# Kernel optimization log

Hardware: AMD Instinct MI355X
Metric: run time of the kernel (lower is better)

## Reference

```python
import jax, jax.numpy as jnp
import numpy as np

EMBED_DIM = 1024
N_HEADS = 16
D_HEAD = EMBED_DIM // N_HEADS


def setup_inputs() -> dict:
    key = jax.random.key(0)
    kx, kq, kk, kv = jax.random.split(key, 4)
    x = jax.random.normal(kx, (2, 2048, EMBED_DIM), dtype=jnp.float32)
    Wq = jax.random.normal(kq, (EMBED_DIM, EMBED_DIM), dtype=jnp.float32) * 0.02
    Wk = jax.random.normal(kk, (EMBED_DIM, EMBED_DIM), dtype=jnp.float32) * 0.02
    Wv = jax.random.normal(kv, (EMBED_DIM, EMBED_DIM), dtype=jnp.float32) * 0.02
    return {"x": x, "Wq": Wq, "Wk": Wk, "Wv": Wv}


def reference(x, Wq, Wk, Wv):
    B, N, D = x.shape
    H, Dh = N_HEADS, D_HEAD
    # Fused QKV projections, then split heads: [B, N, D] -> [B, H, N, Dh]
    q = (x @ Wq).reshape(B, N, H, Dh).transpose(0, 2, 1, 3)
    k = (x @ Wk).reshape(B, N, H, Dh).transpose(0, 2, 1, 3)
    v = (x @ Wv).reshape(B, N, H, Dh).transpose(0, 2, 1, 3)
    scale = 1.0 / jnp.sqrt(jnp.asarray(Dh, dtype=x.dtype))
    scores = jnp.einsum("bhqd,bhkd->bhqk", q, k) * scale  # [B, H, N, N]
    attn = jax.nn.softmax(scores, axis=-1)
    out = jnp.einsum("bhqk,bhkd->bhqd", attn, v)  # [B, H, N, Dh]
    return out.transpose(0, 2, 1, 3).reshape(B, N, D)
```

## Files before the change

kernel.cpp:

```cpp
#include <hip/hip_runtime.h>
#include <cstdint>

typedef __bf16 bf16;
typedef __bf16 bf16x4 __attribute__((ext_vector_type(4)));
typedef __bf16 bf16x8 __attribute__((ext_vector_type(8)));
typedef float floatx4 __attribute__((ext_vector_type(4)));

typedef const __attribute__((address_space(1))) void* as1_cvptr;
typedef __attribute__((address_space(3))) void* as3_vptr;

__device__ __forceinline__ void gl_lds16(const void* g, void* l) {
  __builtin_amdgcn_global_load_lds((as1_cvptr)(uintptr_t)g,
                                   (as3_vptr)(uint32_t)(uintptr_t)l, 16, 0, 0);
}

#define EMBED 1024
#define SEQ 2048
#define NH 16
#define DH 64
#define QSCALE 0.18033688f

__global__ __launch_bounds__(256) void prep(
    const float* __restrict__ x, const float* __restrict__ Wq,
    const float* __restrict__ Wk, const float* __restrict__ Wv,
    bf16* __restrict__ xb, bf16* __restrict__ Wqt,
    bf16* __restrict__ Wkt, bf16* __restrict__ Wvt) {
  __shared__ __align__(16) bf16 tile[64][72];
  int z = blockIdx.y;
  int t = threadIdx.x;
  if (z == 3) {
    size_t base = ((size_t)blockIdx.x * 256 + t) * 8;
#pragma unroll
    for (int it = 0; it < 8; ++it) {
      size_t i = base + (size_t)it * (256 * 256 * 8);
      floatx4 a = *(const floatx4*)(x + i);
      floatx4 bv = *(const floatx4*)(x + i + 4);
      bf16x8 o;
#pragma unroll
      for (int j = 0; j < 4; ++j) { o[j] = (bf16)a[j]; o[4 + j] = (bf16)bv[j]; }
      *(bf16x8*)(xb + i) = o;
    }
    return;
  }
  const float* W = (z == 0) ? Wq : (z == 1) ? Wk : Wv;
  bf16* Wt = (z == 0) ? Wqt : (z == 1) ? Wkt : Wvt;
  int k0 = (blockIdx.x >> 4) * 64, n0 = (blockIdx.x & 15) * 64;
  int r = t >> 3, c = (t & 7) * 8;
#pragma unroll
  for (int half = 0; half < 2; ++half) {
    const float* src = &W[(size_t)(k0 + r + half * 32) * EMBED + n0 + c];
    floatx4 f0 = *(const floatx4*)src;
    floatx4 f1 = *(const floatx4*)(src + 4);
    bf16x8 o;
#pragma unroll
    for (int j = 0; j < 4; ++j) { o[j] = (bf16)f0[j]; o[4 + j] = (bf16)f1[j]; }
    *(bf16x8*)&tile[r + half * 32][c] = o;
  }
  __syncthreads();
#pragma unroll
  for (int p = 0; p < 2; ++p) {
    int nn = (t >> 3) + p * 32, kk = (t & 7) * 8;
    bf16x8 v;
#pragma unroll
    for (int i = 0; i < 8; ++i) v[i] = tile[kk + i][nn];
    *(bf16x8*)&Wt[(size_t)(n0 + nn) * EMBED + k0 + kk] = v;
  }
}

__global__ __launch_bounds__(256) void qkv3(
    const bf16* __restrict__ Xb, const bf16* __restrict__ Wqt,
    const bf16* __restrict__ Wkt, const bf16* __restrict__ Wvt,
    bf16* __restrict__ qo, bf16* __restrict__ ko, bf16* __restrict__ vto) {
  __shared__ __align__(16) bf16 As[128 * 32];
  __shared__ __align__(16) bf16 Bs[128 * 32];

  int gid = blockIdx.x;
  int z = gid % 3;
  int rem = gid / 3;
  int bxx = rem & 7, byy = rem >> 3;

  const bf16* Wt = (z == 0) ? Wqt : (z == 1) ? Wkt : Wvt;
  bf16* out = (z == 0) ? qo : (z == 1) ? ko : vto;
  int m0 = (z == 2 ? bxx : byy) * 128;
  int n0 = (z == 2 ? byy : bxx) * 128;
  const bf16* Asrc = (z == 2) ? Wt : Xb;
  const bf16* Bsrc = (z == 2) ? Xb : Wt;
  float oscale = (z == 0) ? QSCALE : 1.0f;

  int t = threadIdx.x;
  int w = t >> 6, lane = t & 63, ln = lane & 15, quad = lane >> 4;
  int wm = (w >> 1) * 64, wn = (w & 1) * 64;

  floatx4 acc[4][4];
#pragma unroll
  for (int i = 0; i < 4; ++i)
#pragma unroll
    for (int j = 0; j < 4; ++j) acc[i][j] = floatx4{0.f, 0.f, 0.f, 0.f};

  int sr = t >> 2, sc = (t & 3) * 8;
  const bf16* ag = Asrc + (size_t)(m0 + sr) * EMBED + sc;
  const bf16* bg = Bsrc + (size_t)(n0 + sr) * EMBED + sc;
  bf16* al = As + sr * 32 + sc;
  bf16* bl = Bs + sr * 32 + sc;

  for (int k0 = 0; k0 < EMBED; k0 += 32) {
    __syncthreads();
    gl_lds16(ag + k0, al);
    gl_lds16(ag + k0 + (size_t)64 * EMBED, al + 64 * 32);
    gl_lds16(bg + k0, bl);
    gl_lds16(bg + k0 + (size_t)64 * EMBED, bl + 64 * 32);
    __syncthreads();

    bf16x8 afr[4], bfr[4];
#pragma unroll
    for (int i = 0; i < 4; ++i)
      afr[i] = *(const bf16x8*)&As[(wm + i * 16 + ln) * 32 + quad * 8];
#pragma unroll
    for (int j = 0; j < 4; ++j)
      bfr[j] = *(const bf16x8*)&Bs[(wn + j * 16 + ln) * 32 + quad * 8];
#pragma unroll
    for (int i = 0; i < 4; ++i)
#pragma unroll
      for (int j = 0; j < 4; ++j)
        acc[i][j] =
            __builtin_amdgcn_mfma_f32_16x16x32_bf16(afr[i], bfr[j], acc[i][j], 0, 0, 0);
  }

#pragma unroll
  for (int i = 0; i < 4; ++i) {
#pragma unroll
    for (int r = 0; r < 4; ++r) {
      int row = m0 + wm + i * 16 + quad * 4 + r;
#pragma unroll
      for (int j = 0; j < 4; ++j) {
        int col = n0 + wn + j * 16 + ln;
        float v = acc[i][j][r] * oscale;
        size_t dst;
        if (z != 2) {
          int b = row >> 11, ns = row & 2047, h = col >> 6, d = col & 63;
          dst = ((size_t)((b * NH + h) * SEQ + ns)) * DH + d;
        } else {
          int h = row >> 6, d = row & 63, b = col >> 11, ns = col & 2047;
          dst = ((size_t)((b * NH + h) * DH + d)) * SEQ + ns;
        }
        out[dst] = (bf16)v;
      }
    }
  }
}

__global__ __launch_bounds__(1024, 8) void flash(
    const bf16* __restrict__ Qg, const bf16* __restrict__ Kg,
    const bf16* __restrict__ Vtg, float* __restrict__ Og) {
  __shared__ __align__(16) char smem[73728];
  bf16* Ks = (bf16*)smem;
  bf16* Vs = (bf16*)(smem + 18432);
  bf16* Ps = (bf16*)(smem + 36864);
  float* Om = (float*)smem;
  float* Lm = (float*)(smem + 34816);

  int t = threadIdx.x, w = t >> 6, lane = t & 63, ln = lane & 15, quad = lane >> 4;
  int qg = w >> 1, half = w & 1;
  int bh = blockIdx.y;
  int b = bh >> 4, h = bh & 15;
  const bf16* Q = Qg + (size_t)bh * SEQ * DH;
  const bf16* K = Kg + (size_t)bh * SEQ * DH;
  const bf16* Vt = Vtg + (size_t)bh * DH * SEQ;
  int q0 = blockIdx.x * 128 + qg * 16;

  bf16x8 bq[2];
#pragma unroll
  for (int kc = 0; kc < 2; ++kc)
    bq[kc] = *(const bf16x8*)&Q[(size_t)(q0 + ln) * DH + kc * 32 + quad * 8];

  floatx4 oacc[4];
  float li = 0.f;
#pragma unroll
  for (int dt = 0; dt < 4; ++dt) oacc[dt] = floatx4{0.f, 0.f, 0.f, 0.f};

  int sh = t >> 9, st = t & 511;
  int kr = st >> 3, kcol = (st & 7) * 8;
  const bf16* kg = K + (size_t)(sh * 1024 + kr) * DH + kcol;
  const bf16* vg = Vt + (size_t)kr * SEQ + sh * 1024 + kcol;
  bf16* kl = Ks + sh * (64 * 72) + kr * 72 + kcol;
  bf16* vl = Vs + sh * (64 * 72) + kr * 72 + kcol;

  bf16x8 pk = *(const bf16x8*)(kg);
  bf16x8 pv = *(const bf16x8*)(vg);

  const bf16* Ksh = Ks + half * (64 * 72);
  const bf16* Vsh = Vs + half * (64 * 72);
  bf16* Pw = Ps + w * (16 * 72);

  for (int it = 0; it < 16; ++it) {
    __syncthreads();
    *(bf16x8*)kl = pk;
    *(bf16x8*)vl = pv;
    __syncthreads();

    if (it + 1 < 16) {
      pk = *(const bf16x8*)(kg + (size_t)((it + 1) * 64) * DH);
      pv = *(const bf16x8*)(vg + (it + 1) * 64);
    }

    floatx4 s[4];
#pragma unroll
    for (int nt = 0; nt < 4; ++nt) s[nt] = floatx4{0.f, 0.f, 0.f, 0.f};
#pragma unroll
    for (int kc = 0; kc < 2; ++kc) {
#pragma unroll
      for (int nt = 0; nt < 4; ++nt) {
        bf16x8 ak = *(const bf16x8*)&Ksh[(nt * 16 + ln) * 72 + kc * 32 + quad * 8];
        s[nt] = __builtin_amdgcn_mfma_f32_16x16x32_bf16(ak, bq[kc], s[nt], 0, 0, 0);
      }
    }

#pragma unroll
    for (int nt = 0; nt < 4; ++nt) {
      float p0 = exp2f(s[nt][0]);
      float p1 = exp2f(s[nt][1]);
      float p2 = exp2f(s[nt][2]);
      float p3 = exp2f(s[nt][3]);
      li += (p0 + p1) + (p2 + p3);
      bf16x4 pq = {(bf16)p0, (bf16)p1, (bf16)p2, (bf16)p3};
      *(bf16x4*)&Pw[ln * 72 + nt * 16 + quad * 4] = pq;
    }

#pragma unroll
    for (int kc2 = 0; kc2 < 2; ++kc2) {
      bf16x8 ap = *(const bf16x8*)&Pw[ln * 72 + kc2 * 32 + quad * 8];
#pragma unroll
      for (int dt = 0; dt < 4; ++dt) {
        bf16x8 bv = *(const bf16x8*)&Vsh[(dt * 16 + ln) * 72 + kc2 * 32 + quad * 8];
        oacc[dt] = __builtin_amdgcn_mfma_f32_16x16x32_bf16(ap, bv, oacc[dt], 0, 0, 0);
      }
    }
  }

  __syncthreads();
  li += __shfl_xor(li, 16, 64);
  li += __shfl_xor(li, 32, 64);
  if (quad == 0) Lm[half * 128 + qg * 16 + ln] = li;
  if (half) {
#pragma unroll
    for (int r = 0; r < 4; ++r) {
      int q = qg * 16 + quad * 4 + r;
#pragma unroll
      for (int dt = 0; dt < 4; ++dt) Om[q * 68 + dt * 16 + ln] = oacc[dt][r];
    }
  }
  __syncthreads();
  if (!half) {
#pragma unroll
    for (int r = 0; r < 4; ++r) {
      int qq = qg * 16 + quad * 4 + r;
      float lt = Lm[qq] + Lm[128 + qq];
      float inv = 1.0f / lt;
      int ns = blockIdx.x * 128 + qq;
#pragma unroll
      for (int dt = 0; dt < 4; ++dt) {
        int d = dt * 16 + ln;
        float val = (oacc[dt][r] + Om[qq * 68 + d]) * inv;
        Og[((size_t)(b * SEQ + ns)) * EMBED + h * DH + d] = val;
      }
    }
  }
}

extern "C" void kernel_launch(void* const* d_in, const int* in_sizes, int n_in,
                              void* d_out, int out_size, void* d_ws, size_t ws_size,
                              hipStream_t stream) {
  const int XEL = 2 * 2048 * 1024;
  const float *x, *Wq, *Wk, *Wv;
  if (in_sizes[0] == XEL) {
    x = (const float*)d_in[0];
    Wq = (const float*)d_in[1];
    Wk = (const float*)d_in[2];
    Wv = (const float*)d_in[3];
  } else {
    Wk = (const float*)d_in[0];
    Wq = (const float*)d_in[1];
    Wv = (const float*)d_in[2];
    x = (const float*)d_in[3];
  }
  bf16* ws = (bf16*)d_ws;

  const size_t M1 = 1024 * 1024;
  bf16* q_ws = ws;
  bf16* k_ws = ws + 4 * M1;
  bf16* vt_ws = ws + 8 * M1;
  bf16* wqt = ws + 12 * M1;
  bf16* wkt = ws + 13 * M1;
  bf16* wvt = ws + 14 * M1;
  bf16* xb = ws + 15 * M1;

  prep<<<dim3(256, 4), 256, 0, stream>>>(x, Wq, Wk, Wv, xb, wqt, wkt, wvt);
  qkv3<<<dim3(768), 256, 0, stream>>>(xb, wqt, wkt, wvt, q_ws, k_ws, vt_ws);
  flash<<<dim3(16, 32), 1024, 0, stream>>>(q_ws, k_ws, vt_ws, (float*)d_out);
}
```

Before: 178.2 us.

## Restructure flash kernel around 32x32x16 MFMA with in-register P and 4-way KV split

The attention kernel moves from 16x16x32 to 32x32x16 MFMA tiles. Each wave now handles 32 queries over a quarter of the key sequence. The probability tile stays in registers: it is repacked with permlane32_swap and fed straight into the PV MFMA, so the LDS round trip for P is gone. K/V tiles are double-buffered in a larger 144KB LDS block, which removes one barrier per iteration, and the four split partial outputs are reduced through LDS with vectorised final stores. The cost is lower occupancy from the larger LDS footprint and a serial three-step reduction at the end.

```diff
diff --git a/kernel.cpp b/kernel.cpp
--- a/kernel.cpp
+++ b/kernel.cpp
@@ -5,6 +5,9 @@
 typedef __bf16 bf16x4 __attribute__((ext_vector_type(4)));
 typedef __bf16 bf16x8 __attribute__((ext_vector_type(8)));
 typedef float floatx4 __attribute__((ext_vector_type(4)));
+typedef float f32x16 __attribute__((ext_vector_type(16)));
+typedef unsigned int uint2v __attribute__((ext_vector_type(2)));
+typedef unsigned int uint4v __attribute__((ext_vector_type(4)));
 
 typedef const __attribute__((address_space(1))) void* as1_cvptr;
 typedef __attribute__((address_space(3))) void* as3_vptr;
@@ -19,6 +22,12 @@
 #define NH 16
 #define DH 64
 #define QSCALE 0.18033688f
+
+__device__ __forceinline__ unsigned pk_bf16(float a, float b) {
+  unsigned short ua = __builtin_bit_cast(unsigned short, (bf16)a);
+  unsigned short ub = __builtin_bit_cast(unsigned short, (bf16)b);
+  return (unsigned)ua | ((unsigned)ub << 16);
+}
 
 __global__ __launch_bounds__(256) void prep(
     const float* __restrict__ x, const float* __restrict__ Wq,
@@ -149,121 +158,159 @@
   }
 }
 
-__global__ __launch_bounds__(1024, 8) void flash(
+__global__ __launch_bounds__(1024, 4) void flash(
     const bf16* __restrict__ Qg, const bf16* __restrict__ Kg,
     const bf16* __restrict__ Vtg, float* __restrict__ Og) {
-  __shared__ __align__(16) char smem[73728];
+  __shared__ __align__(16) char smem[147456];
   bf16* Ks = (bf16*)smem;
-  bf16* Vs = (bf16*)(smem + 18432);
-  bf16* Ps = (bf16*)(smem + 36864);
+  bf16* Vs = (bf16*)(smem + 73728);
   float* Om = (float*)smem;
   float* Lm = (float*)(smem + 34816);
 
-  int t = threadIdx.x, w = t >> 6, lane = t & 63, ln = lane & 15, quad = lane >> 4;
-  int qg = w >> 1, half = w & 1;
+  int t = threadIdx.x;
+  int lane = t & 63, w = t >> 6;
+  int col = lane & 31, hi = lane >> 5;
+  int qg = w >> 2, split = w & 3;
   int bh = blockIdx.y;
   int b = bh >> 4, h = bh & 15;
   const bf16* Q = Qg + (size_t)bh * SEQ * DH;
   const bf16* K = Kg + (size_t)bh * SEQ * DH;
   const bf16* Vt = Vtg + (size_t)bh * DH * SEQ;
-  int q0 = blockIdx.x * 128 + qg * 16;
-
-  bf16x8 bq[2];
-#pragma unroll
-  for (int kc = 0; kc < 2; ++kc)
-    bq[kc] = *(const bf16x8*)&Q[(size_t)(q0 + ln) * DH + kc * 32 + quad * 8];
-
-  floatx4 oacc[4];
+  int q0 = blockIdx.x * 128 + qg * 32;
+
+  bf16x8 bq[4];
+#pragma unroll
+  for (int kc = 0; kc < 4; ++kc)
+    bq[kc] = *(const bf16x8*)&Q[(size_t)(q0 + col) * DH + kc * 16 + hi * 8];
+
+  f32x16 oacc[2];
+#pragma unroll
+  for (int m = 0; m < 2; ++m)
+#pragma unroll
+    for (int r = 0; r < 16; ++r) oacc[m][r] = 0.f;
   float li = 0.f;
-#pragma unroll
-  for (int dt = 0; dt < 4; ++dt) oacc[dt] = floatx4{0.f, 0.f, 0.f, 0.f};
-
-  int sh = t >> 9, st = t & 511;
-  int kr = st >> 3, kcol = (st & 7) * 8;
-  const bf16* kg = K + (size_t)(sh * 1024 + kr) * DH + kcol;
-  const bf16* vg = Vt + (size_t)kr * SEQ + sh * 1024 + kcol;
-  bf16* kl = Ks + sh * (64 * 72) + kr * 72 + kcol;
-  bf16* vl = Vs + sh * (64 * 72) + kr * 72 + kcol;
-
-  bf16x8 pk = *(const bf16x8*)(kg);
-  bf16x8 pv = *(const bf16x8*)(vg);
-
-  const bf16* Ksh = Ks + half * (64 * 72);
-  const bf16* Vsh = Vs + half * (64 * 72);
-  bf16* Pw = Ps + w * (16 * 72);
-
-  for (int it = 0; it < 16; ++it) {
-    __syncthreads();
-    *(bf16x8*)kl = pk;
-    *(bf16x8*)vl = pv;
-    __syncthreads();
-
-    if (it + 1 < 16) {
-      pk = *(const bf16x8*)(kg + (size_t)((it + 1) * 64) * DH);
-      pv = *(const bf16x8*)(vg + (it + 1) * 64);
-    }
-
-    floatx4 s[4];
-#pragma unroll
-    for (int nt = 0; nt < 4; ++nt) s[nt] = floatx4{0.f, 0.f, 0.f, 0.f};
-#pragma unroll
-    for (int kc = 0; kc < 2; ++kc) {
-#pragma unroll
-      for (int nt = 0; nt < 4; ++nt) {
-        bf16x8 ak = *(const bf16x8*)&Ksh[(nt * 16 + ln) * 72 + kc * 32 + quad * 8];
-        s[nt] = __builtin_amdgcn_mfma_f32_16x16x32_bf16(ak, bq[kc], s[nt], 0, 0, 0);
+
+  int ss = t >> 8, st = t & 255;
+  int kr = st >> 2, kcol = (st & 3) * 16;
+  const bf16* kg = K + ((size_t)(ss * 512 + kr)) * DH + kcol;
+  const bf16* vg = Vt + (size_t)kr * SEQ + ss * 512 + kcol;
+  bf16* kl = Ks + ss * 4608 + kr * 72 + kcol;
+  bf16* vl = Vs + ss * 4608 + kr * 72 + kcol;
+
+  bf16x8 pk0 = *(const bf16x8*)kg;
+  bf16x8 pk1 = *(const bf16x8*)(kg + 8);
+  bf16x8 pv0 = *(const bf16x8*)vg;
+  bf16x8 pv1 = *(const bf16x8*)(vg + 8);
+
+  const bf16* Kb = Ks + split * 4608;
+  const bf16* Vb = Vs + split * 4608;
+
+  for (int it = 0; it < 8; ++it) {
+    int buf = (it & 1) * 18432;
+    *(bf16x8*)(kl + buf) = pk0;
+    *(bf16x8*)(kl + buf + 8) = pk1;
+    *(bf16x8*)(vl + buf) = pv0;
+    *(bf16x8*)(vl + buf + 8) = pv1;
+    __syncthreads();
+
+    if (it + 1 < 8) {
+      size_t ko = (size_t)(it + 1) * 64 * DH;
+      pk0 = *(const bf16x8*)(kg + ko);
+      pk1 = *(const bf16x8*)(kg + ko + 8);
+      pv0 = *(const bf16x8*)(vg + (it + 1) * 64);
+      pv1 = *(const bf16x8*)(vg + (it + 1) * 64 + 8);
+    }
+    const bf16* Kt = Kb + buf;
+    const bf16* Vtb = Vb + buf;
+
+#pragma unroll
+    for (int mt = 0; mt < 2; ++mt) {
+      f32x16 s;
+#pragma unroll
+      for (int r = 0; r < 16; ++r) s[r] = 0.f;
+#pragma unroll
+      for (int kc = 0; kc < 4; ++kc) {
+        bf16x8 ak = *(const bf16x8*)&Kt[(mt * 32 + col) * 72 + kc * 16 + hi * 8];
+        s = __builtin_amdgcn_mfma_f32_32x32x16_bf16(ak, bq[kc], s, 0, 0, 0);
       }
-    }
-
-#pragma unroll
-    for (int nt = 0; nt < 4; ++nt) {
-      float p0 = exp2f(s[nt][0]);
-      float p1 = exp2f(s[nt][1]);
-      float p2 = exp2f(s[nt][2]);
-      float p3 = exp2f(s[nt][3]);
-      li += (p0 + p1) + (p2 + p3);
-      bf16x4 pq = {(bf16)p0, (bf16)p1, (bf16)p2, (bf16)p3};
-      *(bf16x4*)&Pw[ln * 72 + nt * 16 + quad * 4] = pq;
-    }
-
-#pragma unroll
-    for (int kc2 = 0; kc2 < 2; ++kc2) {
-      bf16x8 ap = *(const bf16x8*)&Pw[ln * 72 + kc2 * 32 + quad * 8];
-#pragma unroll
-      for (int dt = 0; dt < 4; ++dt) {
-        bf16x8 bv = *(const bf16x8*)&Vsh[(dt * 16 + ln) * 72 + kc2 * 32 + quad * 8];
-        oacc[dt] = __builtin_amdgcn_mfma_f32_16x16x32_bf16(ap, bv, oacc[dt], 0, 0, 0);
+#pragma unroll
+      for (int cc = 0; cc < 2; ++cc) {
+        int rb = cc * 8;
+        float e0 = exp2f(s[rb + 0]), e1 = exp2f(s[rb + 1]);
+        float e2 = exp2f(s[rb + 2]), e3 = exp2f(s[rb + 3]);
+        float e4 = exp2f(s[rb + 4]), e5 = exp2f(s[rb + 5]);
+        float e6 = exp2f(s[rb + 6]), e7 = exp2f(s[rb + 7]);
+        li += ((e0 + e1) + (e2 + e3)) + ((e4 + e5) + (e6 + e7));
+        unsigned lo0 = pk_bf16(e0, e1), lo1 = pk_bf16(e2, e3);
+        unsigned h0 = pk_bf16(e4, e5), h1 = pk_bf16(e6, e7);
+        uint2v r02 = __builtin_amdgcn_permlane32_swap(lo0, h0, false, false);
+        uint2v r13 = __builtin_amdgcn_permlane32_swap(lo1, h1, false, false);
+        uint4v uu;
+        uu[0] = r02[0]; uu[1] = r13[0]; uu[2] = r02[1]; uu[3] = r13[1];
+        bf16x8 pb = __builtin_bit_cast(bf16x8, uu);
+
+        int c = mt * 2 + cc;
+        bf16x8 av0 = *(const bf16x8*)&Vtb[(col) * 72 + c * 16 + hi * 8];
+        bf16x8 av1 = *(const bf16x8*)&Vtb[(32 + col) * 72 + c * 16 + hi * 8];
+        oacc[0] = __builtin_amdgcn_mfma_f32_32x32x16_bf16(av0, pb, oacc[0], 0, 0, 0);
+        oacc[1] = __builtin_amdgcn_mfma_f32_32x32x16_bf16(av1, pb, oacc[1], 0, 0, 0);
       }
     }
   }
 
+  li += __shfl_xor(li, 32, 64);
+  if (lane < 32) Lm[split * 128 + qg * 32 + col] = li;
+
+#pragma unroll 1
+  for (int rs = 1; rs < 4; ++rs) {
+    if (split == rs) {
+#pragma unroll
+      for (int m = 0; m < 2; ++m)
+#pragma unroll
+        for (int rr = 0; rr < 4; ++rr) {
+          floatx4 v4;
+#pragma unroll
+          for (int j = 0; j < 4; ++j) v4[j] = oacc[m][rr * 4 + j];
+          *(floatx4*)&Om[(qg * 32 + col) * 68 + m * 32 + rr * 8 + hi * 4] = v4;
+        }
+    }
+    __syncthreads();
+    if (split == 0) {
+#pragma unroll
+      for (int m = 0; m < 2; ++m)
+#pragma unroll
+        for (int rr = 0; rr < 4; ++rr) {
+          floatx4 v4 =
+              *(const floatx4*)&Om[(qg * 32 + col) * 68 + m * 32 + rr * 8 + hi * 4];
+#pragma unroll
+          for (int j = 0; j < 4; ++j) oacc[m][rr * 4 + j] += v4[j];
+        }
+    }
+    __syncthreads();
+  }
+  if (split == 0) {
+#pragma unroll
+    for (int m = 0; m < 2; ++m)
+#pragma unroll
+      for (int rr = 0; rr < 4; ++rr) {
+        floatx4 v4;
+#pragma unroll
+        for (int j = 0; j < 4; ++j) v4[j] = oacc[m][rr * 4 + j];
+        *(floatx4*)&Om[(qg * 32 + col) * 68 + m * 32 + rr * 8 + hi * 4] = v4;
+      }
+  }
   __syncthreads();
-  li += __shfl_xor(li, 16, 64);
-  li += __shfl_xor(li, 32, 64);
-  if (quad == 0) Lm[half * 128 + qg * 16 + ln] = li;
-  if (half) {
-#pragma unroll
-    for (int r = 0; r < 4; ++r) {
-      int q = qg * 16 + quad * 4 + r;
-#pragma unroll
-      for (int dt = 0; dt < 4; ++dt) Om[q * 68 + dt * 16 + ln] = oacc[dt][r];
-    }
-  }
-  __syncthreads();
-  if (!half) {
-#pragma unroll
-    for (int r = 0; r < 4; ++r) {
-      int qq = qg * 16 + quad * 4 + r;
-      float lt = Lm[qq] + Lm[128 + qq];
-      float inv = 1.0f / lt;
-      int ns = blockIdx.x * 128 + qq;
-#pragma unroll
-      for (int dt = 0; dt < 4; ++dt) {
-        int d = dt * 16 + ln;
-        float val = (oacc[dt][r] + Om[qq * 68 + d]) * inv;
-        Og[((size_t)(b * SEQ + ns)) * EMBED + h * DH + d] = val;
-      }
-    }
+
+#pragma unroll
+  for (int rep = 0; rep < 2; ++rep) {
+    int idx = rep * 1024 + t;
+    int q = idx >> 4, dc = (idx & 15) * 4;
+    float lt = Lm[q] + Lm[128 + q] + Lm[256 + q] + Lm[384 + q];
+    float inv = 1.0f / lt;
+    floatx4 ov = *(const floatx4*)&Om[q * 68 + dc];
+    ov[0] *= inv; ov[1] *= inv; ov[2] *= inv; ov[3] *= inv;
+    int ns = blockIdx.x * 128 + q;
+    *(floatx4*)&Og[((size_t)(b * SEQ + ns)) * EMBED + h * DH + dc] = ov;
   }
 }
 
```

Measured after the change: 184.7 us. 3.6% more time.
